# Performance work log

Measured on AMD Instinct MI355X. Metric: run time of the kernel, lower is better.

Reference implementation:

```python
import jax, jax.numpy as jnp
import numpy as np

B, T, D, H = 4, 1024, 1024, 16
DK = D // H
SCALE = float(np.sqrt(DK))


def setup_inputs() -> dict:
    key = jax.random.key(0)
    ks = jax.random.split(key, 12)
    std = 1.0 / np.sqrt(D)
    inp = {
        "x": jax.random.normal(ks[0], (B, T, D), dtype=jnp.float32),
        "s2_distances": jax.random.uniform(ks[1], (B, T, T), dtype=jnp.float32),
        # causal mask: 1 where attention allowed (j <= i)
        "mask": jnp.broadcast_to(jnp.tril(jnp.ones((T, T), dtype=jnp.int32)), (B, T, T)),
        "Wq": jax.random.uniform(ks[2], (D, D), jnp.float32, -std, std),
        "bq": jax.random.uniform(ks[3], (D,), jnp.float32, -std, std),
        "Wk": jax.random.uniform(ks[4], (D, D), jnp.float32, -std, std),
        "bk": jax.random.uniform(ks[5], (D,), jnp.float32, -std, std),
        "Wv": jax.random.uniform(ks[6], (D, D), jnp.float32, -std, std),
        "bv": jax.random.uniform(ks[7], (D,), jnp.float32, -std, std),
        "Wo": jax.random.uniform(ks[8], (D, D), jnp.float32, -std, std),
        "bo": jax.random.uniform(ks[9], (D,), jnp.float32, -std, std),
        "spatial_weight": jnp.float32(0.5),
    }
    return inp


def reference(x, s2_distances, mask, Wq, bq, Wk, bk, Wv, bv, Wo, bo, spatial_weight):
    b, t, _ = x.shape
    # projections: torch nn.Linear is x @ W.T + b
    def proj(W, bias):
        y = jnp.einsum("btd,ed->bte", x, W) + bias
        return y.reshape(b, t, H, DK).transpose(0, 2, 1, 3)  # [B,H,T,dk]

    Q, K, V = proj(Wq, bq), proj(Wk, bk), proj(Wv, bv)
    # scores: QK^T/sqrt(dk) - |alpha| * dist  (dist broadcast over heads)
    scores = jnp.einsum("bhqd,bhkd->bhqk", Q, K) / SCALE
    scores = scores - jnp.abs(spatial_weight) * s2_distances[:, None, :, :]
    scores = jnp.where(mask[:, None, :, :] == 0, -jnp.inf, scores)
    probs = jax.nn.softmax(scores, axis=-1)
    out = jnp.einsum("bhqk,bhkd->bhqd", probs, V)
    out = out.transpose(0, 2, 1, 3).reshape(b, t, D)
    return jnp.einsum("btd,ed->bte", out, Wo) + bo
```

## Files before the change

### kernel.cpp

```cpp
#include <hip/hip_runtime.h>
#include <stdint.h>

#define Tt 1024
#define Dd 1024
#define Hh 16

typedef unsigned short u16;
typedef __attribute__((ext_vector_type(8))) short short8;
typedef __attribute__((ext_vector_type(4))) float f32x4;
typedef __attribute__((ext_vector_type(4))) unsigned short u16x4;

typedef const __attribute__((address_space(1))) uint32_t* gptr_t;
typedef __attribute__((address_space(3))) uint32_t* lptr_t;

#define QSCALE 0.18033688011112042f
#define LOG2E 1.4426950408889634f

static __device__ __forceinline__ u16 f2bf(float f) {
  union { float f; unsigned u; } x;
  x.f = f;
  unsigned u = x.u;
  return (u16)((u + 0x7fffu + ((u >> 16) & 1u)) >> 16);
}

static __device__ __forceinline__ u16 f2bf_fast(float f) {
  union { float f; unsigned u; } x;
  x.f = f;
  return (u16)((x.u + 0x8000u) >> 16);
}

static __device__ __forceinline__ float fexp2(float x) {
#if __has_builtin(__builtin_amdgcn_exp2f)
  return __builtin_amdgcn_exp2f(x);
#else
  return exp2f(x);
#endif
}

__global__ __launch_bounds__(256) void cvt_kernel(
    const float* __restrict__ x, const float* __restrict__ wq,
    const float* __restrict__ wk, const float* __restrict__ wv,
    const float* __restrict__ wo, u16* __restrict__ xb, u16* __restrict__ wb) {
  size_t i = ((size_t)blockIdx.x * 256 + threadIdx.x) * 4;
  const size_t XN = (size_t)4 * 1024 * 1024;
  const float* src;
  u16* dst;
  size_t off;
  if (i < XN) {
    src = x; dst = xb; off = i;
  } else {
    size_t j = i - XN;
    int wi = (int)(j >> 20);
    src = (wi == 0) ? wq : (wi == 1) ? wk : (wi == 2) ? wv : wo;
    dst = wb + ((size_t)wi << 20);
    off = j & ((1u << 20) - 1);
  }
  float4 v = *(const float4*)(src + off);
  u16x4 o;
  o.x = f2bf(v.x); o.y = f2bf(v.y); o.z = f2bf(v.z); o.w = f2bf(v.w);
  *(u16x4*)(dst + off) = o;
}

__global__ __launch_bounds__(512, 2) void qkv_fused_kernel(
    const u16* __restrict__ xb, const u16* __restrict__ wb,
    const float* __restrict__ bq, const float* __restrict__ bk,
    const float* __restrict__ bv, u16* __restrict__ Q, u16* __restrict__ Kk,
    u16* __restrict__ Vt) {
  __shared__ u16 lds[65536];
  const int bid = blockIdx.x;
  const int mt = bid & 15, ny = bid >> 4;
  const int z = ny >> 2;
  const int m0 = mt * 256, nc = (ny & 3) * 256;
  const u16* W = wb + ((size_t)z << 20);

  const int t = threadIdx.x, w = t >> 6, l = t & 63;
  const int quad = l >> 4, l15 = l & 15;
  const int wr = w >> 2, wn = w & 3;
  char* ldc = (char*)lds;

  const int srow = w * 16 + ((l >> 3) & 7);
  const int schunk = ((l & 7) ^ ((l >> 3) & 7)) * 8;
  const u16* gA = xb + (size_t)(m0 + srow) * Dd + schunk;
  const u16* gB = W + (size_t)(nc + srow) * Dd + schunk;

  auto stage = [&](int kt, int h) {
    const size_t ro = (size_t)(h * 128) * Dd + (size_t)kt * 64;
    char* base = ldc + ((((kt & 1) << 1) | h) * 32768) + w * 2048;
#pragma unroll
    for (int i = 0; i < 2; i++) {
      __builtin_amdgcn_global_load_lds((gptr_t)(gA + ro + (size_t)i * 8 * Dd),
                                       (lptr_t)(base + i * 1024), 16, 0, 0);
      __builtin_amdgcn_global_load_lds((gptr_t)(gB + ro + (size_t)i * 8 * Dd),
                                       (lptr_t)(base + 16384 + i * 1024), 16, 0, 0);
    }
  };

  f32x4 acc[8][4];
#pragma unroll
  for (int i = 0; i < 8; i++)
#pragma unroll
    for (int j = 0; j < 4; j++) acc[i][j] = (f32x4){0.f, 0.f, 0.f, 0.f};

  stage(0, 0); stage(0, 1);
  stage(1, 0); stage(1, 1);
  asm volatile("s_waitcnt vmcnt(8)" ::: "memory");
  __builtin_amdgcn_s_barrier();

  const int swl = l15 & 7;

#pragma unroll 1
  for (int kt = 0; kt < 16; kt++) {
    const char* slA = ldc + ((((kt & 1) << 1) | wr) * 32768);
    const char* slB = ldc + ((((kt & 1) << 1) | (wn >> 1)) * 32768) + 16384;
    const int rB = (wn & 1) * 64;
    {
      short8 af[8], bfv[4];
      const int cs = ((0 * 4 + quad) ^ swl) * 16;
#pragma unroll
      for (int mi = 0; mi < 8; mi++)
        af[mi] = *(const short8*)(slA + (mi * 16 + l15) * 128 + cs);
#pragma unroll
      for (int ni = 0; ni < 4; ni++)
        bfv[ni] = *(const short8*)(slB + (rB + ni * 16 + l15) * 128 + cs);
      __builtin_amdgcn_s_barrier();
      asm volatile("s_waitcnt lgkmcnt(0)" ::: "memory");
      __builtin_amdgcn_sched_barrier(0);
      __builtin_amdgcn_s_setprio(1);
#pragma unroll
      for (int mi = 0; mi < 8; mi++)
#pragma unroll
        for (int ni = 0; ni < 4; ni++)
          acc[mi][ni] = __builtin_amdgcn_mfma_f32_16x16x32_bf16(
              af[mi], bfv[ni], acc[mi][ni], 0, 0, 0);
      __builtin_amdgcn_s_setprio(0);
    }
    {
      short8 af[8], bfv[4];
      const int cs = ((1 * 4 + quad) ^ swl) * 16;
#pragma unroll
      for (int mi = 0; mi < 8; mi++)
        af[mi] = *(const short8*)(slA + (mi * 16 + l15) * 128 + cs);
#pragma unroll
      for (int ni = 0; ni < 4; ni++)
        bfv[ni] = *(const short8*)(slB + (rB + ni * 16 + l15) * 128 + cs);
      __builtin_amdgcn_s_barrier();
      if (kt + 2 < 16) { stage(kt + 2, 0); stage(kt + 2, 1); }
      asm volatile("s_waitcnt lgkmcnt(0)" ::: "memory");
      __builtin_amdgcn_sched_barrier(0);
      __builtin_amdgcn_s_setprio(1);
#pragma unroll
      for (int mi = 0; mi < 8; mi++)
#pragma unroll
        for (int ni = 0; ni < 4; ni++)
          acc[mi][ni] = __builtin_amdgcn_mfma_f32_16x16x32_bf16(
              af[mi], bfv[ni], acc[mi][ni], 0, 0, 0);
      __builtin_amdgcn_s_setprio(0);
      if (kt < 14) {
        asm volatile("s_waitcnt vmcnt(8)" ::: "memory");
      } else if (kt == 14) {
        asm volatile("s_waitcnt vmcnt(0)" ::: "memory");
      }
      if (kt < 15) __builtin_amdgcn_s_barrier();
    }
  }

  const float* bias = (z == 0) ? bq : (z == 1) ? bk : bv;
  const float scl = (z == 0) ? QSCALE : 1.0f;
  if (z < 2) {
#pragma unroll
    for (int mi = 0; mi < 8; mi++)
#pragma unroll
      for (int ni = 0; ni < 4; ni++) {
        const int n = wn * 64 + ni * 16 + l15;
        const float bn = bias[nc + n];
        const int nsw = n ^ (quad << 4);
#pragma unroll
        for (int r = 0; r < 4; r++) {
          const int m = wr * 128 + mi * 16 + quad * 4 + r;
          lds[m * 256 + nsw] = f2bf((acc[mi][ni][r] + bn) * scl);
        }
      }
  } else {
#pragma unroll
    for (int mi = 0; mi < 8; mi++)
#pragma unroll
      for (int ni = 0; ni < 4; ni++) {
        const int n = wn * 64 + ni * 16 + l15;
        const float bn = bias[nc + n];
        u16x4 o;
        o.x = f2bf(acc[mi][ni][0] + bn);
        o.y = f2bf(acc[mi][ni][1] + bn);
        o.z = f2bf(acc[mi][ni][2] + bn);
        o.w = f2bf(acc[mi][ni][3] + bn);
        const int mp = (wr * 128 + mi * 16 + quad * 4) ^ ((n & 7) * 8);
        *(u16x4*)&lds[n * 256 + mp] = o;
      }
  }
  __syncthreads();
  const int row = t >> 5;
  const int c8 = (t & 31) * 8;
  if (z < 2) {
    u16* out = (z == 0) ? Q : Kk;
#pragma unroll
    for (int it = 0; it < 16; it++) {
      const int rr = it * 16 + row;
      const int pos = c8 ^ ((((rr >> 2) & 3)) << 4);
      *(short8*)(out + (size_t)(m0 + rr) * Dd + nc + c8) =
          *(const short8*)&lds[rr * 256 + pos];
    }
  } else {
    const int b2 = m0 >> 10, t0 = m0 & (Tt - 1);
#pragma unroll
    for (int it = 0; it < 16; it++) {
      const int rr = it * 16 + row;
      const int pos = c8 ^ ((rr & 7) * 8);
      *(short8*)(Vt + ((size_t)b2 * Dd + nc + rr) * Tt + t0 + c8) =
          *(const short8*)&lds[rr * 256 + pos];
    }
  }
}

__global__ __launch_bounds__(512) void gemm_out_kernel(
    const u16* __restrict__ Ao, const u16* __restrict__ Wo,
    const float* __restrict__ bo, float* __restrict__ out) {
  __shared__ u16 lds[32768];
  const int mt = blockIdx.x & 31, ny = blockIdx.x >> 5;
  const int m0 = mt * 128, n0 = ny * 128;
  const int t = threadIdx.x, w = t >> 6, l = t & 63;
  const int quad = l >> 4, l15 = l & 15;
  const int wr = w >> 2, wn = w & 3;
  char* ldc = (char*)lds;

  const int srow = w * 8 + (l >> 3);
  const int schunk = ((l & 7) ^ ((l >> 3) & 7)) * 8;
  const u16* gA = Ao + (size_t)(m0 + srow) * Dd + schunk;
  const u16* gB = Wo + (size_t)(n0 + srow) * Dd + schunk;

  auto stage = [&](int kt) {
    char* base = ldc + (kt & 1) * 32768 + w * 1024;
#pragma unroll
    for (int i = 0; i < 2; i++) {
      __builtin_amdgcn_global_load_lds(
          (gptr_t)(gA + (size_t)i * 64 * Dd + (size_t)kt * 64),
          (lptr_t)(base + i * 8192), 16, 0, 0);
      __builtin_amdgcn_global_load_lds(
          (gptr_t)(gB + (size_t)i * 64 * Dd + (size_t)kt * 64),
          (lptr_t)(base + 16384 + i * 8192), 16, 0, 0);
    }
  };

  f32x4 acc[4][2];
#pragma unroll
  for (int i = 0; i < 4; i++)
#pragma unroll
    for (int j = 0; j < 2; j++) acc[i][j] = (f32x4){0.f, 0.f, 0.f, 0.f};

  stage(0); stage(1);
  asm volatile("s_waitcnt vmcnt(4)" ::: "memory");
  __builtin_amdgcn_s_barrier();

  const int swl = l15 & 7;

#pragma unroll 1
  for (int kt = 0; kt < 16; kt++) {
    const char* sl = ldc + (kt & 1) * 32768;
    short8 af[2][4], bfv[2][2];
#pragma unroll
    for (int ks = 0; ks < 2; ks++) {
      const int cs = ((ks * 4 + quad) ^ swl) * 16;
#pragma unroll
      for (int mi = 0; mi < 4; mi++)
        af[ks][mi] = *(const short8*)(sl + (wr * 64 + mi * 16 + l15) * 128 + cs);
#pragma unroll
      for (int ni = 0; ni < 2; ni++)
        bfv[ks][ni] = *(const short8*)(sl + 16384 + (wn * 32 + ni * 16 + l15) * 128 + cs);
    }
    __builtin_amdgcn_s_barrier();
    if (kt + 2 < 16) stage(kt + 2);
    asm volatile("s_waitcnt lgkmcnt(0)" ::: "memory");
    __builtin_amdgcn_sched_barrier(0);
    __builtin_amdgcn_s_setprio(1);
#pragma unroll
    for (int ks = 0; ks < 2; ks++)
#pragma unroll
      for (int mi = 0; mi < 4; mi++)
#pragma unroll
        for (int ni = 0; ni < 2; ni++)
          acc[mi][ni] = __builtin_amdgcn_mfma_f32_16x16x32_bf16(
              af[ks][mi], bfv[ks][ni], acc[mi][ni], 0, 0, 0);
    __builtin_amdgcn_s_setprio(0);
    if (kt < 14) {
      asm volatile("s_waitcnt vmcnt(4)" ::: "memory");
    } else if (kt == 14) {
      asm volatile("s_waitcnt vmcnt(0)" ::: "memory");
    }
    if (kt < 15) __builtin_amdgcn_s_barrier();
  }

#pragma unroll
  for (int mi = 0; mi < 4; mi++)
#pragma unroll
    for (int ni = 0; ni < 2; ni++) {
      const int n = n0 + wn * 32 + ni * 16 + l15;
      const float bn = bo[n];
#pragma unroll
      for (int r = 0; r < 4; r++) {
        const int m = m0 + wr * 64 + mi * 16 + quad * 4 + r;
        out[(size_t)m * Dd + n] = acc[mi][ni][r] + bn;
      }
    }
}

__global__ __launch_bounds__(256) void attn_kernel(
    const u16* __restrict__ Q, const u16* __restrict__ Kk,
    const u16* __restrict__ Vt, const float* __restrict__ dist,
    const float* __restrict__ alphap, u16* __restrict__ Oo) {
  __shared__ u16 lK[2][64 * 64];
  __shared__ u16 lV[2][64 * 64];
  __shared__ u16 lPp[4][16 * 64];
  const int t = threadIdx.x, w = t >> 6, l = t & 63, quad = l >> 4, l15 = l & 15;
  const int g = blockIdx.x >> 8;
  const int j = (blockIdx.x >> 6) & 3;
  const int bh = blockIdx.x & 63;
  const int qb = (g == 0) ? 15 - j : (g == 1) ? 8 + j : (g == 2) ? 7 - j : j;
  const int h = bh & (Hh - 1), b = bh >> 4;
  const int q0 = qb * 64;
  const float scl = -fabsf(alphap[0]) * LOG2E;

  const int srow = w * 8 + (l >> 3);
  const int schunk = ((l & 7) ^ ((l >> 3) & 7)) * 8;
  const u16* gK = Kk + ((size_t)b * Tt + srow) * Dd + h * 64 + schunk;
  const u16* gV = Vt + ((size_t)b * Dd + h * 64 + srow) * Tt + schunk;
  char* lKc0 = (char*)&lK[0][0];
  char* lVc0 = (char*)&lV[0][0];
  const int wbase = w * 1024;

  auto stage = [&](int k0, int buf) {
#pragma unroll
    for (int i = 0; i < 2; i++) {
      __builtin_amdgcn_global_load_lds(
          (gptr_t)(gK + (size_t)(k0 + i * 32) * Dd),
          (lptr_t)(lKc0 + buf * 8192 + wbase + i * 4096), 16, 0, 0);
      __builtin_amdgcn_global_load_lds(
          (gptr_t)(gV + (size_t)(i * 32) * Tt + k0),
          (lptr_t)(lVc0 + buf * 8192 + wbase + i * 4096), 16, 0, 0);
    }
  };

  const int qrow = q0 + w * 16 + l15;
  const u16* Qp = Q + ((size_t)b * Tt + qrow) * Dd + h * 64 + quad * 8;
  const short8 qf0 = *(const short8*)Qp;
  const short8 qf1 = *(const short8*)(Qp + 32);
  const float* bp = dist + ((size_t)b * Tt + qrow) * Tt + quad * 4;

  const int xr = l15 & 7;
  u16* lpr = &lPp[w][l15 * 64];
  const int niter = qb + 1;

  f32x4 oacc[4];
#pragma unroll
  for (int dt = 0; dt < 4; dt++) oacc[dt] = (f32x4){0.f, 0.f, 0.f, 0.f};
  f32x4 lsum4 = (f32x4){0.f, 0.f, 0.f, 0.f};
  f32x4 bbA[4], bbB[4], bbC[4];

  stage(0, 0);
#pragma unroll
  for (int nt = 0; nt < 4; nt++) bbA[nt] = *(const f32x4*)(bp + nt * 16);
  if (niter > 1) {
#pragma unroll
    for (int nt = 0; nt < 4; nt++) bbB[nt] = *(const f32x4*)(bp + 64 + nt * 16);
  } else {
#pragma unroll
    for (int nt = 0; nt < 4; nt++) bbB[nt] = bbA[nt];
  }

#pragma unroll 1
  for (int kt = 0; kt < niter; kt++) {
    const int buf = kt & 1;
    if (kt + 1 < niter) {
      asm volatile("s_waitcnt vmcnt(4)" ::: "memory");
    } else {
      asm volatile("s_waitcnt vmcnt(0)" ::: "memory");
    }
    __builtin_amdgcn_s_barrier();
    if (kt + 1 < niter) stage((kt + 1) * 64, buf ^ 1);
    if (kt + 2 < niter) {
#pragma unroll
      for (int nt = 0; nt < 4; nt++)
        bbC[nt] = *(const f32x4*)(bp + (kt + 2) * 64 + nt * 16);
    }
    f32x4 sacc[4];
#pragma unroll
    for (int nt = 0; nt < 4; nt++) {
#pragma unroll
      for (int r = 0; r < 4; r++) sacc[nt][r] = scl * bbA[nt][r];
    }
#pragma unroll
    for (int ks = 0; ks < 2; ks++) {
      const short8 qf = ks ? qf1 : qf0;
      const int cs = ((ks * 4 + quad) ^ xr) * 8;
#pragma unroll
      for (int nt = 0; nt < 4; nt++) {
        const short8 kf = *(const short8*)&lK[buf][(nt * 16 + l15) * 64 + cs];
        sacc[nt] = __builtin_amdgcn_mfma_f32_16x16x32_bf16(kf, qf, sacc[nt], 0, 0, 0);
      }
    }
    if (kt == qb) {
      const int kbase = kt * 64 + quad * 4;
#pragma unroll
      for (int nt = 0; nt < 4; nt++) {
        u16x4 pk;
#pragma unroll
        for (int r = 0; r < 4; r++) {
          const float p = (kbase + nt * 16 + r <= qrow) ? fexp2(sacc[nt][r]) : 0.f;
          lsum4[nt] += p;
          pk[r] = f2bf_fast(p);
        }
        *(u16x4*)&lpr[((nt * 4 + quad) ^ (xr << 1)) * 4] = pk;
      }
    } else {
#pragma unroll
      for (int nt = 0; nt < 4; nt++) {
        u16x4 pk;
#pragma unroll
        for (int r = 0; r < 4; r++) {
          const float p = fexp2(sacc[nt][r]);
          lsum4[nt] += p;
          pk[r] = f2bf_fast(p);
        }
        *(u16x4*)&lpr[((nt * 4 + quad) ^ (xr << 1)) * 4] = pk;
      }
    }
#pragma unroll
    for (int ks = 0; ks < 2; ks++) {
      const int cs = ((ks * 4 + quad) ^ xr) * 8;
      const short8 pa = *(const short8*)&lpr[cs];
#pragma unroll
      for (int dt = 0; dt < 4; dt++) {
        const short8 vf = *(const short8*)&lV[buf][(dt * 16 + l15) * 64 + cs];
        oacc[dt] = __builtin_amdgcn_mfma_f32_16x16x32_bf16(pa, vf, oacc[dt], 0, 0, 0);
      }
    }
#pragma unroll
    for (int nt = 0; nt < 4; nt++) { bbA[nt] = bbB[nt]; bbB[nt] = bbC[nt]; }
  }

  float lsum = (lsum4[0] + lsum4[1]) + (lsum4[2] + lsum4[3]);
  lsum += __shfl_xor(lsum, 16);
  lsum += __shfl_xor(lsum, 32);
  const float inv = 1.0f / lsum;
  float invq[4];
#pragma unroll
  for (int r = 0; r < 4; r++) invq[r] = __shfl(inv, quad * 4 + r);
#pragma unroll
  for (int dt = 0; dt < 4; dt++) {
#pragma unroll
    for (int r = 0; r < 4; r++) {
      Oo[((size_t)b * Tt + q0 + w * 16 + quad * 4 + r) * Dd + h * 64 + dt * 16 + l15] =
          f2bf(oacc[dt][r] * invq[r]);
    }
  }
}

extern "C" void kernel_launch(void* const* d_in, const int* in_sizes, int n_in,
                              void* d_out, int out_size, void* d_ws, size_t ws_size,
                              hipStream_t stream) {
  const float* x = (const float*)d_in[0];
  const float* dist = (const float*)d_in[1];
  const float* Wq = (const float*)d_in[3];
  const float* bq = (const float*)d_in[4];
  const float* Wk = (const float*)d_in[5];
  const float* bk = (const float*)d_in[6];
  const float* Wv = (const float*)d_in[7];
  const float* bv = (const float*)d_in[8];
  const float* Wo = (const float*)d_in[9];
  const float* bo = (const float*)d_in[10];
  const float* alphap = (const float*)d_in[11];

  char* ws = (char*)d_ws;
  u16* xb = (u16*)(ws);
  u16* wb = (u16*)(ws + ((size_t)8 << 20));
  u16* Qb = (u16*)(ws + ((size_t)16 << 20));
  u16* Kb = (u16*)(ws + ((size_t)24 << 20));
  u16* Vtb = (u16*)(ws + ((size_t)32 << 20));
  u16* Ob = xb;
  float* outp = (float*)d_out;

  cvt_kernel<<<8192, 256, 0, stream>>>(x, Wq, Wk, Wv, Wo, xb, wb);
  qkv_fused_kernel<<<192, 512, 0, stream>>>(xb, wb, bq, bk, bv, Qb, Kb, Vtb);
  attn_kernel<<<1024, 256, 0, stream>>>(Qb, Kb, Vtb, dist, alphap, Ob);
  gemm_out_kernel<<<256, 512, 0, stream>>>(Ob, wb + ((size_t)3 << 20), bo, outp);
}
```

Before: 198.9 us.

## Split QKV GEMM loop into four sub-phases with staggered A/B prefetch and block swizzle

Restructures the QKV projection main loop. The single combined stage is split into separate A and B loads: A is prefetched one k-tile ahead and B two ahead, issued at different points within each iteration. Each k-tile now runs as four smaller 4x4 MFMA sub-phases, halving the A-fragment registers and spreading LDS reads across more barriers. Block IDs are also remapped so neighbouring blocks share x and weight tiles in L2. The cost is more barriers per iteration and finer vmcnt bookkeeping that must stay correct.

After: 196.0 us. About the same (-1.5%).

```diff
diff --git a/kernel.cpp b/kernel.cpp
--- a/kernel.cpp
+++ b/kernel.cpp
@@ -67,8 +67,10 @@
     const float* __restrict__ bv, u16* __restrict__ Q, u16* __restrict__ Kk,
     u16* __restrict__ Vt) {
   __shared__ u16 lds[65536];
-  const int bid = blockIdx.x;
-  const int mt = bid & 15, ny = bid >> 4;
+  const int bid0 = blockIdx.x;
+  const int x8 = bid0 & 7, q = bid0 >> 3;
+  const int mt = (x8 & 3) * 4 + (q & 3);
+  const int ny = (x8 >> 2) * 6 + (q >> 2);
   const int z = ny >> 2;
   const int m0 = mt * 256, nc = (ny & 3) * 256;
   const u16* W = wb + ((size_t)z << 20);
@@ -83,17 +85,30 @@
   const u16* gA = xb + (size_t)(m0 + srow) * Dd + schunk;
   const u16* gB = W + (size_t)(nc + srow) * Dd + schunk;
 
-  auto stage = [&](int kt, int h) {
-    const size_t ro = (size_t)(h * 128) * Dd + (size_t)kt * 64;
-    char* base = ldc + ((((kt & 1) << 1) | h) * 32768) + w * 2048;
-#pragma unroll
-    for (int i = 0; i < 2; i++) {
-      __builtin_amdgcn_global_load_lds((gptr_t)(gA + ro + (size_t)i * 8 * Dd),
-                                       (lptr_t)(base + i * 1024), 16, 0, 0);
-      __builtin_amdgcn_global_load_lds((gptr_t)(gB + ro + (size_t)i * 8 * Dd),
-                                       (lptr_t)(base + 16384 + i * 1024), 16, 0, 0);
+  auto stageA = [&](int kt) {
+    const int p = kt & 1;
+#pragma unroll
+    for (int h = 0; h < 2; h++) {
+      char* base = ldc + (((p << 1) | h) * 32768) + w * 2048;
+      const size_t ro = (size_t)(h * 128) * Dd + (size_t)kt * 64;
+#pragma unroll
+      for (int i = 0; i < 2; i++)
+        __builtin_amdgcn_global_load_lds((gptr_t)(gA + ro + (size_t)i * 8 * Dd),
+                                         (lptr_t)(base + i * 1024), 16, 0, 0);
     }
   };
+  auto stageB = [&](int kt) {
+    const int p = kt & 1;
+#pragma unroll
+    for (int h = 0; h < 2; h++) {
+      char* base = ldc + (((p << 1) | h) * 32768) + 16384 + w * 2048;
+      const size_t ro = (size_t)(h * 128) * Dd + (size_t)kt * 64;
+#pragma unroll
+      for (int i = 0; i < 2; i++)
+        __builtin_amdgcn_global_load_lds((gptr_t)(gB + ro + (size_t)i * 8 * Dd),
+                                         (lptr_t)(base + i * 1024), 16, 0, 0);
+    }
+  };
 
   f32x4 acc[8][4];
 #pragma unroll
@@ -101,67 +116,98 @@
 #pragma unroll
     for (int j = 0; j < 4; j++) acc[i][j] = (f32x4){0.f, 0.f, 0.f, 0.f};
 
-  stage(0, 0); stage(0, 1);
-  stage(1, 0); stage(1, 1);
-  asm volatile("s_waitcnt vmcnt(8)" ::: "memory");
+  stageA(0); stageB(0); stageB(1);
+  asm volatile("s_waitcnt vmcnt(4)" ::: "memory");
   __builtin_amdgcn_s_barrier();
 
   const int swl = l15 & 7;
 
 #pragma unroll 1
   for (int kt = 0; kt < 16; kt++) {
-    const char* slA = ldc + ((((kt & 1) << 1) | wr) * 32768);
-    const char* slB = ldc + ((((kt & 1) << 1) | (wn >> 1)) * 32768) + 16384;
+    const int p = kt & 1;
+    const char* sA = ldc + (((p << 1) | wr) * 32768);
+    const char* sB = ldc + (((p << 1) | (wn >> 1)) * 32768) + 16384;
     const int rB = (wn & 1) * 64;
-    {
-      short8 af[8], bfv[4];
-      const int cs = ((0 * 4 + quad) ^ swl) * 16;
-#pragma unroll
-      for (int mi = 0; mi < 8; mi++)
-        af[mi] = *(const short8*)(slA + (mi * 16 + l15) * 128 + cs);
+    short8 af[4], bfv[4];
+    const int cs0 = (quad ^ swl) * 16;
+    const int cs1 = ((4 + quad) ^ swl) * 16;
+
+#pragma unroll
+    for (int mi = 0; mi < 4; mi++)
+      af[mi] = *(const short8*)(sA + (mi * 16 + l15) * 128 + cs0);
+#pragma unroll
+    for (int ni = 0; ni < 4; ni++)
+      bfv[ni] = *(const short8*)(sB + (rB + ni * 16 + l15) * 128 + cs0);
+    if (kt + 1 < 16) stageA(kt + 1);
+    __builtin_amdgcn_s_barrier();
+    asm volatile("s_waitcnt lgkmcnt(0)" ::: "memory");
+    __builtin_amdgcn_sched_barrier(0);
+    __builtin_amdgcn_s_setprio(1);
+#pragma unroll
+    for (int mi = 0; mi < 4; mi++)
 #pragma unroll
       for (int ni = 0; ni < 4; ni++)
-        bfv[ni] = *(const short8*)(slB + (rB + ni * 16 + l15) * 128 + cs);
-      __builtin_amdgcn_s_barrier();
-      asm volatile("s_waitcnt lgkmcnt(0)" ::: "memory");
-      __builtin_amdgcn_sched_barrier(0);
-      __builtin_amdgcn_s_setprio(1);
-#pragma unroll
-      for (int mi = 0; mi < 8; mi++)
-#pragma unroll
-        for (int ni = 0; ni < 4; ni++)
-          acc[mi][ni] = __builtin_amdgcn_mfma_f32_16x16x32_bf16(
-              af[mi], bfv[ni], acc[mi][ni], 0, 0, 0);
-      __builtin_amdgcn_s_setprio(0);
-    }
-    {
-      short8 af[8], bfv[4];
-      const int cs = ((1 * 4 + quad) ^ swl) * 16;
-#pragma unroll
-      for (int mi = 0; mi < 8; mi++)
-        af[mi] = *(const short8*)(slA + (mi * 16 + l15) * 128 + cs);
+        acc[mi][ni] = __builtin_amdgcn_mfma_f32_16x16x32_bf16(
+            af[mi], bfv[ni], acc[mi][ni], 0, 0, 0);
+    __builtin_amdgcn_s_setprio(0);
+    __builtin_amdgcn_s_barrier();
+
+#pragma unroll
+    for (int mi = 0; mi < 4; mi++)
+      af[mi] = *(const short8*)(sA + ((mi + 4) * 16 + l15) * 128 + cs0);
+    __builtin_amdgcn_s_barrier();
+    asm volatile("s_waitcnt lgkmcnt(0)" ::: "memory");
+    __builtin_amdgcn_sched_barrier(0);
+    __builtin_amdgcn_s_setprio(1);
+#pragma unroll
+    for (int mi = 0; mi < 4; mi++)
 #pragma unroll
       for (int ni = 0; ni < 4; ni++)
-        bfv[ni] = *(const short8*)(slB + (rB + ni * 16 + l15) * 128 + cs);
-      __builtin_amdgcn_s_barrier();
-      if (kt + 2 < 16) { stage(kt + 2, 0); stage(kt + 2, 1); }
-      asm volatile("s_waitcnt lgkmcnt(0)" ::: "memory");
-      __builtin_amdgcn_sched_barrier(0);
-      __builtin_amdgcn_s_setprio(1);
-#pragma unroll
-      for (int mi = 0; mi < 8; mi++)
-#pragma unroll
-        for (int ni = 0; ni < 4; ni++)
-          acc[mi][ni] = __builtin_amdgcn_mfma_f32_16x16x32_bf16(
-              af[mi], bfv[ni], acc[mi][ni], 0, 0, 0);
-      __builtin_amdgcn_s_setprio(0);
-      if (kt < 14) {
-        asm volatile("s_waitcnt vmcnt(8)" ::: "memory");
-      } else if (kt == 14) {
-        asm volatile("s_waitcnt vmcnt(0)" ::: "memory");
-      }
-      if (kt < 15) __builtin_amdgcn_s_barrier();
-    }
+        acc[mi + 4][ni] = __builtin_amdgcn_mfma_f32_16x16x32_bf16(
+            af[mi], bfv[ni], acc[mi + 4][ni], 0, 0, 0);
+    __builtin_amdgcn_s_setprio(0);
+    __builtin_amdgcn_s_barrier();
+
+#pragma unroll
+    for (int mi = 0; mi < 4; mi++)
+      af[mi] = *(const short8*)(sA + (mi * 16 + l15) * 128 + cs1);
+#pragma unroll
+    for (int ni = 0; ni < 4; ni++)
+      bfv[ni] = *(const short8*)(sB + (rB + ni * 16 + l15) * 128 + cs1);
+    __builtin_amdgcn_s_barrier();
+    asm volatile("s_waitcnt lgkmcnt(0)" ::: "memory");
+    __builtin_amdgcn_sched_barrier(0);
+    __builtin_amdgcn_s_setprio(1);
+#pragma unroll
+    for (int mi = 0; mi < 4; mi++)
+#pragma unroll
+      for (int ni = 0; ni < 4; ni++)
+        acc[mi][ni] = __builtin_amdgcn_mfma_f32_16x16x32_bf16(
+            af[mi], bfv[ni], acc[mi][ni], 0, 0, 0);
+    __builtin_amdgcn_s_setprio(0);
+    __builtin_amdgcn_s_barrier();
+
+#pragma unroll
+    for (int mi = 0; mi < 4; mi++)
+      af[mi] = *(const short8*)(sA + ((mi + 4) * 16 + l15) * 128 + cs1);
+    if (kt + 2 < 16) stageB(kt + 2);
+    __builtin_amdgcn_s_barrier();
+    asm volatile("s_waitcnt lgkmcnt(0)" ::: "memory");
+    __builtin_amdgcn_sched_barrier(0);
+    __builtin_amdgcn_s_setprio(1);
+#pragma unroll
+    for (int mi = 0; mi < 4; mi++)
+#pragma unroll
+      for (int ni = 0; ni < 4; ni++)
+        acc[mi + 4][ni] = __builtin_amdgcn_mfma_f32_16x16x32_bf16(
+            af[mi], bfv[ni], acc[mi + 4][ni], 0, 0, 0);
+    __builtin_amdgcn_s_setprio(0);
+    if (kt < 14) {
+      asm volatile("s_waitcnt vmcnt(4)" ::: "memory");
+    } else if (kt == 14) {
+      asm volatile("s_waitcnt vmcnt(0)" ::: "memory");
+    }
+    __builtin_amdgcn_s_barrier();
   }
 
   const float* bias = (z == 0) ? bq : (z == 1) ? bk : bv;
```
